# Optimization experiments

Hardware: AMD Instinct MI355X
Metric: run time of the kernel (lower is better)

The kernel has to match this reference:

```python
import jax, jax.numpy as jnp
import numpy as np

# Config: b=2, n=1024, dim=512, heads=8, dim_head=64, L=8 slices/head, temperature=0.1

def setup_inputs() -> dict:
    key = jax.random.key(0)
    ks = jax.random.split(key, 5)
    b, n, dim = 2, 1024, 512
    heads, dim_head, L = 8, 64, 8
    inner = heads * dim_head
    x = jax.random.normal(ks[0], (b, n, dim), jnp.float32)
    W_qkv = jax.random.normal(ks[1], (dim, 3 * inner), jnp.float32) * 0.02
    theta = jax.random.normal(ks[2], (heads, L, dim_head), jnp.float32)
    W_out = jax.random.normal(ks[3], (inner, dim), jnp.float32) * 0.02
    b_out = jnp.zeros((dim,), jnp.float32)
    return {"x": x, "W_qkv": W_qkv, "theta": theta, "W_out": W_out, "b_out": b_out}


def reference(x, W_qkv, theta, W_out, b_out):
    b, n, dim = x.shape
    heads, L, dim_head = theta.shape
    scale = dim_head ** -0.5
    temperature = 0.1
    # QKV projection (no bias) and head split: b n (h d) -> b h n d
    qkv = x @ W_qkv
    q, k, v = jnp.split(qkv, 3, axis=-1)
    sh = lambda t: t.reshape(b, n, heads, dim_head).transpose(0, 2, 1, 3)
    q = sh(q) * scale
    k = sh(k) * scale
    v = sh(v)
    # Esp: learnable unit slice directions per head, 1D projections
    th = theta / jnp.linalg.norm(theta, axis=-1, keepdims=True)  # [h, L, d]
    qp = jnp.einsum('bhnd,hld->bhln', q, th)  # [b,h,L,n]
    kp = jnp.einsum('bhnd,hld->bhln', k, th)
    # per-slice soft 1D transport plan (rows sum to 1), averaged over slices,
    # scaled to total-mass-1 plan (rows sum 1/n)
    d2 = (qp[..., :, None] - kp[..., None, :]) ** 2  # [b,h,L,n,n]
    plans = jax.nn.softmax(-d2 / temperature, axis=-1)
    P = plans.mean(axis=2) / n  # [b,h,n,n], rows sum to 1/n
    # SA: attn = attn * attn.shape[-1] -> row-stochastic
    attn = P * n
    out = jnp.einsum('bhnm,bhmd->bhnd', attn, v)
    out = out.transpose(0, 2, 1, 3).reshape(b, n, heads * dim_head)
    out = out @ W_out + b_out  # to_out Linear (dropout=0 in eval)
    return out, attn
```

## Files before the change

kernel.cpp:

```cpp
#include <hip/hip_runtime.h>
#include <hip/hip_bf16.h>

#define CEXP (-14.4269504088896340736f)

typedef __attribute__((ext_vector_type(8))) short bfrag8;
typedef __attribute__((ext_vector_type(4))) float fvec4;
typedef __attribute__((ext_vector_type(8))) unsigned short ushort8;
typedef __attribute__((ext_vector_type(4))) unsigned short ushort4v;

__device__ inline unsigned short f2bf(float f) {
    unsigned u = __builtin_bit_cast(unsigned, f);
    u += 0x7fffu + ((u >> 16) & 1u);
    return (unsigned short)(u >> 16);
}
__device__ inline float bf2f(unsigned short h) {
    unsigned u = ((unsigned)h) << 16;
    return __builtin_bit_cast(float, u);
}

template <int CTRL, int RMASK>
__device__ __forceinline__ float dpp_add(float v) {
    int m = __builtin_amdgcn_update_dpp(0, __builtin_bit_cast(int, v), CTRL, RMASK, 0xf, true);
    return v + __builtin_bit_cast(float, m);
}
__device__ __forceinline__ float wave_sum64(float v) {
    v = dpp_add<0xB1,  0xf>(v);
    v = dpp_add<0x4E,  0xf>(v);
    v = dpp_add<0x141, 0xf>(v);
    v = dpp_add<0x140, 0xf>(v);
    v = dpp_add<0x142, 0xa>(v);
    v = dpp_add<0x143, 0xc>(v);
    return __builtin_bit_cast(float, __builtin_amdgcn_readlane(__builtin_bit_cast(int, v), 63));
}

__global__ __launch_bounds__(256) void k_wproj(const float* __restrict__ Wqkv,
                                               const float* __restrict__ theta,
                                               const float* __restrict__ Wout,
                                               const float* __restrict__ x,
                                               float* __restrict__ Wqp,
                                               float* __restrict__ Wkp,
                                               float* __restrict__ Wv,
                                               unsigned short* __restrict__ WoThi,
                                               unsigned short* __restrict__ WoTlo,
                                               unsigned short* __restrict__ xhi,
                                               unsigned short* __restrict__ xlo) {
    __shared__ float th_s[64 * 65];
    __shared__ float ts2[64 * 65];
    int tid = threadIdx.x;
    int hl = tid & 63, cl = tid >> 6;
    #pragma unroll
    for (int i = 0; i < 16; ++i) {
        int r = cl * 16 + i;
        th_s[r * 65 + hl] = theta[r * 64 + hl];
    }
    __syncthreads();
    const float* ts = th_s + hl * 65;
    float ss = 0.f;
    #pragma unroll 8
    for (int d = 0; d < 64; ++d) ss = fmaf(ts[d], ts[d], ss);
    float inv = rsqrtf(ss);
    int c = blockIdx.x * 4 + cl;
    int h = hl >> 3;
    const float* wq = Wqkv + c * 1536 + h * 64;
    const float* wk = wq + 512;
    float aq = 0.f, ak = 0.f;
    #pragma unroll 4
    for (int d = 0; d < 64; ++d) {
        float tv = ts[d];
        aq = fmaf(wq[d], tv, aq);
        ak = fmaf(wk[d], tv, ak);
    }
    Wqp[c * 64 + hl] = aq * inv;
    Wkp[c * 64 + hl] = ak * inv;

    int c0b = blockIdx.x * 4;
    const float4* src = (const float4*)(Wqkv + 1024);
    float4* dst = (float4*)Wv;
    #pragma unroll
    for (int j = 0; j < 2; ++j) {
        int idx = j * 256 + tid;
        int cr = c0b + (idx >> 7), o4 = idx & 127;
        dst[cr * 128 + o4] = src[cr * 384 + o4];
    }

    {
        const float4* x4 = (const float4*)x;
        int base4 = blockIdx.x * 2048;
        #pragma unroll
        for (int j = 0; j < 8; ++j) {
            int idx = base4 + j * 256 + tid;
            float4 v = x4[idx];
            float vv[4] = {v.x, v.y, v.z, v.w};
            ushort4v h4, l4;
            #pragma unroll
            for (int jj = 0; jj < 4; ++jj) {
                unsigned short hi = f2bf(vv[jj]);
                h4[jj] = hi;
                l4[jj] = f2bf(vv[jj] - bf2f(hi));
            }
            *(ushort4v*)(xhi + (size_t)idx * 4) = h4;
            *(ushort4v*)(xlo + (size_t)idx * 4) = l4;
        }
    }

    if (blockIdx.x < 64) {
        int r0 = (blockIdx.x >> 3) * 64;
        int c0 = (blockIdx.x & 7) * 64;
        int cc = tid & 63, rr = tid >> 6;
        #pragma unroll
        for (int k = 0; k < 16; ++k) {
            int r = rr + 4 * k;
            ts2[r * 65 + cc] = Wout[(r0 + r) * 512 + c0 + cc];
        }
        __syncthreads();
        int kk = tid & 63, nn = tid >> 6;
        #pragma unroll
        for (int i = 0; i < 16; ++i) {
            int n = nn + 4 * i;
            float v = ts2[kk * 65 + n];
            unsigned short hi = f2bf(v);
            WoThi[(size_t)(c0 + n) * 512 + r0 + kk] = hi;
            WoTlo[(size_t)(c0 + n) * 512 + r0 + kk] = f2bf(v - bf2f(hi));
        }
    }
}

__global__ __launch_bounds__(256) void k_wsplit(const float* __restrict__ Wqp,
                                                const float* __restrict__ Wkp,
                                                const float* __restrict__ Wv,
                                                unsigned short* __restrict__ WThi,
                                                unsigned short* __restrict__ WTlo) {
    __shared__ float ts[64 * 65];
    int blk = blockIdx.x;
    const float* src;
    int ld, k0, nbase;
    if (blk < 8)       { src = Wqp + blk * 64 * 64;       ld = 64;  k0 = blk * 64;       nbase = 0; }
    else if (blk < 16) { src = Wkp + (blk - 8) * 64 * 64; ld = 64;  k0 = (blk - 8) * 64; nbase = 64; }
    else {
        int t = blk - 16, kt = t >> 3, nt = t & 7;
        src = Wv + kt * 64 * 512 + nt * 64;  ld = 512; k0 = kt * 64; nbase = 128 + nt * 64;
    }
    int tid = threadIdx.x;
    int cc = tid & 63, rr = tid >> 6;
    #pragma unroll
    for (int k = 0; k < 16; ++k) {
        int r = rr + 4 * k;
        ts[r * 65 + cc] = src[r * ld + cc];
    }
    __syncthreads();
    int kk = tid & 63, nn = tid >> 6;
    #pragma unroll
    for (int i = 0; i < 16; ++i) {
        int n = nn + 4 * i;
        float v = ts[kk * 65 + n];
        unsigned short hi = f2bf(v);
        WThi[(size_t)(nbase + n) * 512 + k0 + kk] = hi;
        WTlo[(size_t)(nbase + n) * 512 + k0 + kk] = f2bf(v - bf2f(hi));
    }
}

__global__ __launch_bounds__(256) void k_proj(const unsigned short* __restrict__ xhi,
                                              const unsigned short* __restrict__ xlo,
                                              const unsigned short* __restrict__ WThi,
                                              const unsigned short* __restrict__ WTlo,
                                              float* __restrict__ qp,
                                              float* __restrict__ kp,
                                              unsigned short* __restrict__ vThi,
                                              unsigned short* __restrict__ vTlo) {
    __shared__ unsigned short ps[32 * 512];
    int blk = blockIdx.x;
    int cs = blk % 5;
    int rg = blk / 5;
    int tid = threadIdx.x;
    int w = tid >> 6, lane = tid & 63;

    const ushort8* xh8 = (const ushort8*)(xhi + (size_t)rg * 16 * 512);
    const ushort8* xl8 = (const ushort8*)(xlo + (size_t)rg * 16 * 512);
    #pragma unroll
    for (int rep = 0; rep < 4; ++rep) {
        int idx = rep * 256 + tid;
        int row = idx >> 6, c8 = (idx & 63) * 8;
        int swz = (row & 7) << 3;
        *(ushort8*)(ps + row * 512 + (c8 ^ swz))        = xh8[idx];
        *(ushort8*)(ps + (row + 16) * 512 + (c8 ^ swz)) = xl8[idx];
    }
    __syncthreads();

    int ar  = lane & 15;
    int asw = (ar & 7) << 3;
    int ak  = (lane >> 4) * 8;
    const unsigned short* aph = ps + ar * 512;
    const unsigned short* apl = ps + (ar + 16) * 512;
    int colb = cs * 128 + w * 32;
    size_t b0 = (size_t)(colb + ar) * 512 + ak;
    size_t b1 = b0 + 16 * 512;
    fvec4 acc0 = {0.f, 0.f, 0.f, 0.f};
    fvec4 acc1 = {0.f, 0.f, 0.f, 0.f};
    #pragma unroll 4
    for (int s = 0; s < 16; ++s) {
        int ko = s * 32 + ak;
        bfrag8 ahi = *(const bfrag8*)(aph + (ko ^ asw));
        bfrag8 alo = *(const bfrag8*)(apl + (ko ^ asw));
        bfrag8 bh0 = *(const bfrag8*)(WThi + b0 + s * 32);
        bfrag8 bl0 = *(const bfrag8*)(WTlo + b0 + s * 32);
        bfrag8 bh1 = *(const bfrag8*)(WThi + b1 + s * 32);
        bfrag8 bl1 = *(const bfrag8*)(WTlo + b1 + s * 32);
        acc0 = __builtin_amdgcn_mfma_f32_16x16x32_bf16(ahi, bh0, acc0, 0, 0, 0);
        acc0 = __builtin_amdgcn_mfma_f32_16x16x32_bf16(ahi, bl0, acc0, 0, 0, 0);
        acc0 = __builtin_amdgcn_mfma_f32_16x16x32_bf16(alo, bh0, acc0, 0, 0, 0);
        acc1 = __builtin_amdgcn_mfma_f32_16x16x32_bf16(ahi, bh1, acc1, 0, 0, 0);
        acc1 = __builtin_amdgcn_mfma_f32_16x16x32_bf16(ahi, bl1, acc1, 0, 0, 0);
        acc1 = __builtin_amdgcn_mfma_f32_16x16x32_bf16(alo, bh1, acc1, 0, 0, 0);
    }

    int rowb = rg * 16 + (lane >> 4) * 4;
    int b = rowb >> 10, n = rowb & 1023;
    fvec4 accs[2] = {acc0, acc1};
    #pragma unroll
    for (int t = 0; t < 2; ++t) {
        int col = colb + t * 16 + ar;
        fvec4 a = accs[t];
        if (col < 128) {
            int hl = col & 63;
            float* dstp = (col < 64) ? qp : kp;
            fvec4 st;
            st[0] = a[0] * 0.125f; st[1] = a[1] * 0.125f;
            st[2] = a[2] * 0.125f; st[3] = a[3] * 0.125f;
            *(fvec4*)(dstp + ((size_t)((b * 8 + (hl >> 3)) * 8 + (hl & 7))) * 1024 + n) = st;
        } else {
            int vcol = col - 128;
            int h = vcol >> 6, d = vcol & 63;
            ushort4v h4, l4;
            #pragma unroll
            for (int q = 0; q < 4; ++q) {
                unsigned short hi = f2bf(a[q]);
                h4[q] = hi;
                l4[q] = f2bf(a[q] - bf2f(hi));
            }
            size_t off = (size_t)(b * 8 + h) * 65536 + (size_t)d * 1024 + n;
            *(ushort4v*)(vThi + off) = h4;
            *(ushort4v*)(vTlo + off) = l4;
        }
    }
}

__global__ __launch_bounds__(512) void k_attn_pv(const float* __restrict__ qp,
                                                 const float* __restrict__ kp,
                                                 const unsigned short* __restrict__ vThi,
                                                 const unsigned short* __restrict__ vTlo,
                                                 float* __restrict__ attn,
                                                 float* __restrict__ oh) {
    __shared__ float s_buf[8 * 1024];
    __shared__ float sc[4 * 64 * 4];
    int bx = blockIdx.x;
    int idx = bx >> 3;
    int bh = (bx & 7) * 2 + (idx >> 7);
    int rowbase = (idx & 127) * 8;
    int tid = threadIdx.x;
    int w = tid >> 6, lane = tid & 63;

    const float4* kp4 = (const float4*)(kp + bh * 8192);
    float4* kps4 = (float4*)s_buf;
    #pragma unroll
    for (int k = 0; k < 4; ++k) kps4[k * 512 + tid] = kp4[k * 512 + tid];

    int r = rowbase + w;
    float qv[8];
    #pragma unroll
    for (int l = 0; l < 8; ++l) qv[l] = qp[bh * 8192 + l * 1024 + r];
    __syncthreads();

    const fvec4 CE4 = {CEXP, CEXP, CEXP, CEXP};
    fvec4 acc4[4];
    #pragma unroll
    for (int mm = 0; mm < 4; ++mm) acc4[mm] = (fvec4){0.f, 0.f, 0.f, 0.f};

    for (int l = 0; l < 8; ++l) {
        fvec4 kv4[4], e4[4];
        #pragma unroll
        for (int mm = 0; mm < 4; ++mm)
            kv4[mm] = *(const fvec4*)(s_buf + l * 1024 + mm * 256 + lane * 4);
        float sqs = -2.f * CEXP * qv[l];
        fvec4 sq4 = {sqs, sqs, sqs, sqs};
        fvec4 sum4 = {0.f, 0.f, 0.f, 0.f};
        #pragma unroll
        for (int mm = 0; mm < 4; ++mm) {
            fvec4 k2 = (kv4[mm] * kv4[mm]) * CE4;
            fvec4 t  = sq4 * kv4[mm] + k2;
            fvec4 e;
            e[0] = __builtin_amdgcn_exp2f(t[0]);
            e[1] = __builtin_amdgcn_exp2f(t[1]);
            e[2] = __builtin_amdgcn_exp2f(t[2]);
            e[3] = __builtin_amdgcn_exp2f(t[3]);
            e4[mm] = e;
            sum4 += e;
        }
        float s = (sum4[0] + sum4[1]) + (sum4[2] + sum4[3]);
        float inv = 0.125f * __builtin_amdgcn_rcpf(wave_sum64(s));
        fvec4 inv4 = {inv, inv, inv, inv};
        #pragma unroll
        for (int mm = 0; mm < 4; ++mm) acc4[mm] = e4[mm] * inv4 + acc4[mm];
    }

    __syncthreads();

    unsigned short* ps = (unsigned short*)s_buf;
    int swz = w << 3;
    #pragma unroll
    for (int mm = 0; mm < 4; ++mm) {
        ushort4v h4, l4;
        #pragma unroll
        for (int jj = 0; jj < 4; ++jj) {
            float v = acc4[mm][jj];
            unsigned short hi = f2bf(v);
            h4[jj] = hi;
            l4[jj] = f2bf(v - bf2f(hi));
        }
        int j0 = mm * 256 + lane * 4;
        *(ushort4v*)(ps + w * 1024 + (j0 ^ swz))       = h4;
        *(ushort4v*)(ps + (w + 8) * 1024 + (j0 ^ swz)) = l4;
    }
    __syncthreads();

    float* aR = attn + ((size_t)(bh * 1024 + r)) * 1024;
    #pragma unroll
    for (int mm = 0; mm < 4; ++mm)
        __builtin_nontemporal_store(acc4[mm], (fvec4*)(aR + mm * 256 + lane * 4));

    int n0 = (w & 3) * 16;
    int kh = w >> 2;
    int ar  = lane & 15;
    int asw = (ar & 7) << 3;
    int ak  = (lane >> 4) * 8;
    const unsigned short* ap = ps + ar * 1024;
    size_t boff = (size_t)bh * 65536 + (size_t)(n0 + (lane & 15)) * 1024 + ak;
    const unsigned short* bh_p = vThi + boff;
    const unsigned short* bl_p = vTlo + boff;
    fvec4 c2 = {0.f, 0.f, 0.f, 0.f};
    #pragma unroll 4
    for (int s = kh * 16; s < kh * 16 + 16; ++s) {
        bfrag8 a  = *(const bfrag8*)(ap + ((s * 32 + ak) ^ asw));
        bfrag8 vh = *(const bfrag8*)(bh_p + s * 32);
        bfrag8 vl = *(const bfrag8*)(bl_p + s * 32);
        c2 = __builtin_amdgcn_mfma_f32_16x16x32_bf16(a, vh, c2, 0, 0, 0);
        c2 = __builtin_amdgcn_mfma_f32_16x16x32_bf16(a, vl, c2, 0, 0, 0);
    }
    if (w >= 4) {
        #pragma unroll
        for (int q = 0; q < 4; ++q) sc[(w - 4) * 256 + lane * 4 + q] = c2[q];
    }
    __syncthreads();
    if (w < 4) {
        int b = bh >> 3, h = bh & 7;
        #pragma unroll
        for (int q = 0; q < 4; ++q) {
            float t = c2[q] + sc[w * 256 + lane * 4 + q];
            t += __shfl_xor(t, 32);
            if (lane < 32) {
                int row = rowbase + (lane >> 4) * 4 + q;
                oh[(b * 1024 + row) * 512 + h * 64 + n0 + (lane & 15)] = t;
            }
        }
    }
}

__global__ __launch_bounds__(256) void k_out(const float* __restrict__ oh,
                                             const unsigned short* __restrict__ WoThi,
                                             const unsigned short* __restrict__ WoTlo,
                                             const float* __restrict__ bout,
                                             float* __restrict__ out) {
    __shared__ unsigned short ps[32 * 512];
    int blk = blockIdx.x;
    int cs = blk & 3;
    int rg = blk >> 2;
    int tid = threadIdx.x;
    int w = tid >> 6, lane = tid & 63;

    const float4* og = (const float4*)(oh + (size_t)rg * 16 * 512);
    #pragma unroll
    for (int rep = 0; rep < 8; ++rep) {
        int idx = rep * 256 + tid;
        int row = idx >> 7, c4 = idx & 127;
        float4 v = og[idx];
        int swz = (row & 7) << 3;
        int cbase = c4 * 4;
        ushort4v h4, l4;
        float vv[4] = {v.x, v.y, v.z, v.w};
        #pragma unroll
        for (int jj = 0; jj < 4; ++jj) {
            unsigned short hi = f2bf(vv[jj]);
            h4[jj] = hi;
            l4[jj] = f2bf(vv[jj] - bf2f(hi));
        }
        *(ushort4v*)(ps + row * 512 + (cbase ^ swz))        = h4;
        *(ushort4v*)(ps + (row + 16) * 512 + (cbase ^ swz)) = l4;
    }
    __syncthreads();

    int ar  = lane & 15;
    int asw = (ar & 7) << 3;
    int ak  = (lane >> 4) * 8;
    const unsigned short* aph = ps + ar * 512;
    const unsigned short* apl = ps + (ar + 16) * 512;
    int colb = cs * 128 + w * 32;
    size_t b0 = (size_t)(colb + ar) * 512 + ak;
    size_t b1 = b0 + 16 * 512;
    fvec4 acc0 = {0.f, 0.f, 0.f, 0.f};
    fvec4 acc1 = {0.f, 0.f, 0.f, 0.f};
    #pragma unroll 4
    for (int s = 0; s < 16; ++s) {
        int ko = s * 32 + ak;
        bfrag8 ahi = *(const bfrag8*)(aph + (ko ^ asw));
        bfrag8 alo = *(const bfrag8*)(apl + (ko ^ asw));
        bfrag8 bh0 = *(const bfrag8*)(WoThi + b0 + s * 32);
        bfrag8 bl0 = *(const bfrag8*)(WoTlo + b0 + s * 32);
        bfrag8 bh1 = *(const bfrag8*)(WoThi + b1 + s * 32);
        bfrag8 bl1 = *(const bfrag8*)(WoTlo + b1 + s * 32);
        acc0 = __builtin_amdgcn_mfma_f32_16x16x32_bf16(ahi, bh0, acc0, 0, 0, 0);
        acc0 = __builtin_amdgcn_mfma_f32_16x16x32_bf16(ahi, bl0, acc0, 0, 0, 0);
        acc0 = __builtin_amdgcn_mfma_f32_16x16x32_bf16(alo, bh0, acc0, 0, 0, 0);
        acc1 = __builtin_amdgcn_mfma_f32_16x16x32_bf16(ahi, bh1, acc1, 0, 0, 0);
        acc1 = __builtin_amdgcn_mfma_f32_16x16x32_bf16(ahi, bl1, acc1, 0, 0, 0);
        acc1 = __builtin_amdgcn_mfma_f32_16x16x32_bf16(alo, bh1, acc1, 0, 0, 0);
    }
    int rowb = rg * 16 + (lane >> 4) * 4;
    int col0 = colb + ar;
    float bias0 = bout[col0], bias1 = bout[col0 + 16];
    #pragma unroll
    for (int q = 0; q < 4; ++q) {
        out[(rowb + q) * 512 + col0]      = acc0[q] + bias0;
        out[(rowb + q) * 512 + col0 + 16] = acc1[q] + bias1;
    }
}

extern "C" void kernel_launch(void* const* d_in, const int* in_sizes, int n_in,
                              void* d_out, int out_size, void* d_ws, size_t ws_size,
                              hipStream_t stream) {
    const float* x     = (const float*)d_in[0];
    const float* Wqkv  = (const float*)d_in[1];
    const float* theta = (const float*)d_in[2];
    const float* Wout  = (const float*)d_in[3];
    const float* bout  = (const float*)d_in[4];

    float* out  = (float*)d_out;
    float* attn = out + 2 * 1024 * 512;

    float* ws  = (float*)d_ws;
    float* Wqp = ws;
    float* Wkp = ws + 32768;
    float* qp  = ws + 65536;
    float* kp  = ws + 196608;
    unsigned short* vThi = (unsigned short*)(ws + 327680);
    unsigned short* vTlo = (unsigned short*)(ws + 851968);
    float* oh   = ws + 1376256;
    unsigned short* xhi = (unsigned short*)(ws + 1376256);
    unsigned short* xlo = (unsigned short*)(ws + 1900544);
    float* Wv   = ws + 2424832;
    unsigned short* WoThi = (unsigned short*)(ws + 2686976);
    unsigned short* WoTlo = (unsigned short*)(ws + 2818048);
    unsigned short* WThi  = (unsigned short*)(ws + 2949120);
    unsigned short* WTlo  = (unsigned short*)(ws + 3112960);

    k_wproj   <<<128,  256, 0, stream>>>(Wqkv, theta, Wout, x, Wqp, Wkp, Wv, WoThi, WoTlo, xhi, xlo);
    k_wsplit  <<<80,   256, 0, stream>>>(Wqp, Wkp, Wv, WThi, WTlo);
    k_proj    <<<640,  256, 0, stream>>>(xhi, xlo, WThi, WTlo, qp, kp, vThi, vTlo);
    k_attn_pv <<<2048, 512, 0, stream>>>(qp, kp, vThi, vTlo, attn, oh);
    k_out     <<<512,  256, 0, stream>>>(oh, WoThi, WoTlo, bout, out);
}
```

Before: 131.7 us.

## Fuse weight bf16 split into wproj kernel and emit split attention output

```diff
diff --git a/kernel.cpp b/kernel.cpp
--- a/kernel.cpp
+++ b/kernel.cpp
@@ -37,15 +37,17 @@
                                                const float* __restrict__ theta,
                                                const float* __restrict__ Wout,
                                                const float* __restrict__ x,
-                                               float* __restrict__ Wqp,
-                                               float* __restrict__ Wkp,
-                                               float* __restrict__ Wv,
+                                               unsigned short* __restrict__ WThi,
+                                               unsigned short* __restrict__ WTlo,
                                                unsigned short* __restrict__ WoThi,
                                                unsigned short* __restrict__ WoTlo,
                                                unsigned short* __restrict__ xhi,
                                                unsigned short* __restrict__ xlo) {
     __shared__ float th_s[64 * 65];
     __shared__ float ts2[64 * 65];
+    __shared__ float tq[4][64];
+    __shared__ float tk[4][64];
+    __shared__ float wvs[4][512];
     int tid = threadIdx.x;
     int hl = tid & 63, cl = tid >> 6;
     #pragma unroll
@@ -59,7 +61,8 @@
     #pragma unroll 8
     for (int d = 0; d < 64; ++d) ss = fmaf(ts[d], ts[d], ss);
     float inv = rsqrtf(ss);
-    int c = blockIdx.x * 4 + cl;
+    int c0b = blockIdx.x * 4;
+    int c = c0b + cl;
     int h = hl >> 3;
     const float* wq = Wqkv + c * 1536 + h * 64;
     const float* wk = wq + 512;
@@ -70,17 +73,18 @@
         aq = fmaf(wq[d], tv, aq);
         ak = fmaf(wk[d], tv, ak);
     }
-    Wqp[c * 64 + hl] = aq * inv;
-    Wkp[c * 64 + hl] = ak * inv;
-
-    int c0b = blockIdx.x * 4;
-    const float4* src = (const float4*)(Wqkv + 1024);
-    float4* dst = (float4*)Wv;
-    #pragma unroll
-    for (int j = 0; j < 2; ++j) {
-        int idx = j * 256 + tid;
-        int cr = c0b + (idx >> 7), o4 = idx & 127;
-        dst[cr * 128 + o4] = src[cr * 384 + o4];
+    tq[cl][hl] = aq * inv;
+    tk[cl][hl] = ak * inv;
+
+    {
+        const float4* src = (const float4*)(Wqkv + 1024);
+        #pragma unroll
+        for (int j = 0; j < 2; ++j) {
+            int idx = j * 256 + tid;
+            int rloc = idx >> 7, o4 = idx & 127;
+            float4 v = src[(c0b + rloc) * 384 + o4];
+            *(float4*)(&wvs[rloc][o4 * 4]) = v;
+        }
     }
 
     {
@@ -102,6 +106,43 @@
             *(ushort4v*)(xlo + (size_t)idx * 4) = l4;
         }
     }
+    __syncthreads();
+
+    {
+        int n = tid & 63, g = tid >> 6;
+        const float (*tp)[64] = (g < 2) ? tq : tk;
+        float vsrc[4];
+        #pragma unroll
+        for (int j = 0; j < 4; ++j) vsrc[j] = tp[j][n];
+        ushort4v st;
+        if ((g & 1) == 0) {
+            #pragma unroll
+            for (int j = 0; j < 4; ++j) st[j] = f2bf(vsrc[j]);
+        } else {
+            #pragma unroll
+            for (int j = 0; j < 4; ++j) {
+                unsigned short hi = f2bf(vsrc[j]);
+                st[j] = f2bf(vsrc[j] - bf2f(hi));
+            }
+        }
+        unsigned short* base = ((g & 1) == 0) ? WThi : WTlo;
+        int nrow = (g < 2) ? n : (64 + n);
+        *(ushort4v*)(base + (size_t)nrow * 512 + c0b) = st;
+    }
+    #pragma unroll
+    for (int j2 = 0; j2 < 2; ++j2) {
+        int n = j2 * 256 + tid;
+        ushort4v h4, l4;
+        #pragma unroll
+        for (int k = 0; k < 4; ++k) {
+            float v = wvs[k][n];
+            unsigned short hi = f2bf(v);
+            h4[k] = hi;
+            l4[k] = f2bf(v - bf2f(hi));
+        }
+        *(ushort4v*)(WThi + (size_t)(128 + n) * 512 + c0b) = h4;
+        *(ushort4v*)(WTlo + (size_t)(128 + n) * 512 + c0b) = l4;
+    }
 
     if (blockIdx.x < 64) {
         int r0 = (blockIdx.x >> 3) * 64;
@@ -122,40 +163,6 @@
             WoThi[(size_t)(c0 + n) * 512 + r0 + kk] = hi;
             WoTlo[(size_t)(c0 + n) * 512 + r0 + kk] = f2bf(v - bf2f(hi));
         }
-    }
-}
-
-__global__ __launch_bounds__(256) void k_wsplit(const float* __restrict__ Wqp,
-                                                const float* __restrict__ Wkp,
-                                                const float* __restrict__ Wv,
-                                                unsigned short* __restrict__ WThi,
-                                                unsigned short* __restrict__ WTlo) {
-    __shared__ float ts[64 * 65];
-    int blk = blockIdx.x;
-    const float* src;
-    int ld, k0, nbase;
-    if (blk < 8)       { src = Wqp + blk * 64 * 64;       ld = 64;  k0 = blk * 64;       nbase = 0; }
-    else if (blk < 16) { src = Wkp + (blk - 8) * 64 * 64; ld = 64;  k0 = (blk - 8) * 64; nbase = 64; }
-    else {
-        int t = blk - 16, kt = t >> 3, nt = t & 7;
-        src = Wv + kt * 64 * 512 + nt * 64;  ld = 512; k0 = kt * 64; nbase = 128 + nt * 64;
-    }
-    int tid = threadIdx.x;
-    int cc = tid & 63, rr = tid >> 6;
-    #pragma unroll
-    for (int k = 0; k < 16; ++k) {
-        int r = rr + 4 * k;
-        ts[r * 65 + cc] = src[r * ld + cc];
-    }
-    __syncthreads();
-    int kk = tid & 63, nn = tid >> 6;
-    #pragma unroll
-    for (int i = 0; i < 16; ++i) {
-        int n = nn + 4 * i;
-        float v = ts[kk * 65 + n];
-        unsigned short hi = f2bf(v);
-        WThi[(size_t)(nbase + n) * 512 + k0 + kk] = hi;
-        WTlo[(size_t)(nbase + n) * 512 + k0 + kk] = f2bf(v - bf2f(hi));
     }
 }
 
@@ -249,7 +256,8 @@
                                                  const unsigned short* __restrict__ vThi,
                                                  const unsigned short* __restrict__ vTlo,
                                                  float* __restrict__ attn,
-                                                 float* __restrict__ oh) {
+                                                 unsigned short* __restrict__ ohhi,
+                                                 unsigned short* __restrict__ ohlo) {
     __shared__ float s_buf[8 * 1024];
     __shared__ float sc[4 * 64 * 4];
     int bx = blockIdx.x;
@@ -333,7 +341,7 @@
     int asw = (ar & 7) << 3;
     int ak  = (lane >> 4) * 8;
     const unsigned short* ap = ps + ar * 1024;
-    size_t boff = (size_t)bh * 65536 + (size_t)(n0 + (lane & 15)) * 1024 + ak;
+    size_t boff = (size_t)bh * 65536 + (size_t)(n0 + ar) * 1024 + ak;
     const unsigned short* bh_p = vThi + boff;
     const unsigned short* bl_p = vTlo + boff;
     fvec4 c2 = {0.f, 0.f, 0.f, 0.f};
@@ -358,13 +366,17 @@
             t += __shfl_xor(t, 32);
             if (lane < 32) {
                 int row = rowbase + (lane >> 4) * 4 + q;
-                oh[(b * 1024 + row) * 512 + h * 64 + n0 + (lane & 15)] = t;
+                size_t o = (size_t)(b * 1024 + row) * 512 + h * 64 + n0 + ar;
+                unsigned short hi = f2bf(t);
+                ohhi[o] = hi;
+                ohlo[o] = f2bf(t - bf2f(hi));
             }
         }
     }
 }
 
-__global__ __launch_bounds__(256) void k_out(const float* __restrict__ oh,
+__global__ __launch_bounds__(256) void k_out(const unsigned short* __restrict__ ohhi,
+                                             const unsigned short* __restrict__ ohlo,
                                              const unsigned short* __restrict__ WoThi,
                                              const unsigned short* __restrict__ WoTlo,
                                              const float* __restrict__ bout,
@@ -376,24 +388,15 @@
     int tid = threadIdx.x;
     int w = tid >> 6, lane = tid & 63;
 
-    const float4* og = (const float4*)(oh + (size_t)rg * 16 * 512);
-    #pragma unroll
-    for (int rep = 0; rep < 8; ++rep) {
+    const ushort8* ogh = (const ushort8*)(ohhi + (size_t)rg * 16 * 512);
+    const ushort8* ogl = (const ushort8*)(ohlo + (size_t)rg * 16 * 512);
+    #pragma unroll
+    for (int rep = 0; rep < 4; ++rep) {
         int idx = rep * 256 + tid;
-        int row = idx >> 7, c4 = idx & 127;
-        float4 v = og[idx];
+        int row = idx >> 6, c8 = (idx & 63) * 8;
         int swz = (row & 7) << 3;
-        int cbase = c4 * 4;
-        ushort4v h4, l4;
-        float vv[4] = {v.x, v.y, v.z, v.w};
-        #pragma unroll
-        for (int jj = 0; jj < 4; ++jj) {
-            unsigned short hi = f2bf(vv[jj]);
-            h4[jj] = hi;
-            l4[jj] = f2bf(vv[jj] - bf2f(hi));
-        }
-        *(ushort4v*)(ps + row * 512 + (cbase ^ swz))        = h4;
-        *(ushort4v*)(ps + (row + 16) * 512 + (cbase ^ swz)) = l4;
+        *(ushort8*)(ps + row * 512 + (c8 ^ swz))        = ogh[idx];
+        *(ushort8*)(ps + (row + 16) * 512 + (c8 ^ swz)) = ogl[idx];
     }
     __syncthreads();
 
@@ -446,24 +449,21 @@
     float* attn = out + 2 * 1024 * 512;
 
     float* ws  = (float*)d_ws;
-    float* Wqp = ws;
-    float* Wkp = ws + 32768;
     float* qp  = ws + 65536;
     float* kp  = ws + 196608;
     unsigned short* vThi = (unsigned short*)(ws + 327680);
     unsigned short* vTlo = (unsigned short*)(ws + 851968);
-    float* oh   = ws + 1376256;
     unsigned short* xhi = (unsigned short*)(ws + 1376256);
     unsigned short* xlo = (unsigned short*)(ws + 1900544);
-    float* Wv   = ws + 2424832;
+    unsigned short* ohhi = xhi;
+    unsigned short* ohlo = xlo;
     unsigned short* WoThi = (unsigned short*)(ws + 2686976);
     unsigned short* WoTlo = (unsigned short*)(ws + 2818048);
     unsigned short* WThi  = (unsigned short*)(ws + 2949120);
     unsigned short* WTlo  = (unsigned short*)(ws + 3112960);
 
-    k_wproj   <<<128,  256, 0, stream>>>(Wqkv, theta, Wout, x, Wqp, Wkp, Wv, WoThi, WoTlo, xhi, xlo);
-    k_wsplit  <<<80,   256, 0, stream>>>(Wqp, Wkp, Wv, WThi, WTlo);
+    k_wproj   <<<128,  256, 0, stream>>>(Wqkv, theta, Wout, x, WThi, WTlo, WoThi, WoTlo, xhi, xlo);
     k_proj    <<<640,  256, 0, stream>>>(xhi, xlo, WThi, WTlo, qp, kp, vThi, vTlo);
-    k_attn_pv <<<2048, 512, 0, stream>>>(qp, kp, vThi, vTlo, attn, oh);
-    k_out     <<<512,  256, 0, stream>>>(oh, WoThi, WoTlo, bout, out);
-}
+    k_attn_pv <<<2048, 512, 0, stream>>>(qp, kp, vThi, vTlo, attn, ohhi, ohlo);
+    k_out     <<<512,  256, 0, stream>>>(ohhi, ohlo, WoThi, WoTlo, bout, out);
+}
```

Measured after the change: 130.5 us. Within noise of the previous version (-0.9%).
